# Optimization experiments

Measured on AMD Instinct MI355X. Metric: run time of the kernel, lower is better.

The kernel has to match this reference:

```python
import math
import jax, jax.numpy as jnp
import numpy as np

INPUT_DIM = 1024


def setup_inputs() -> dict:
    key = jax.random.key(0)
    k1, k2, k3 = jax.random.split(key, 3)
    x = jax.random.normal(k1, (16, INPUT_DIM, 64, 64), dtype=jnp.float32)
    # Conv2d(input_dim, 1, kernel_size=1): weight [1, C, 1, 1] -> store as [C], bias [1]
    fan_in = INPUT_DIM
    bound = 1.0 / math.sqrt(fan_in)
    key_w = jax.random.uniform(k2, (INPUT_DIM,), minval=-bound, maxval=bound, dtype=jnp.float32)
    key_b = jax.random.uniform(k3, (1,), minval=-bound, maxval=bound, dtype=jnp.float32)
    return {"x": x, "key_w": key_w, "key_b": key_b}


def reference(x, key_w, key_b):
    B, C, H, W = x.shape
    scale = 1.0 / math.sqrt(C)
    # 1x1 conv C->1 == channel contraction; logits over spatial positions
    logits = (jnp.einsum('bchw,c->bhw', x, key_w) + key_b[0]) * scale  # [B,H,W]
    attn = jax.nn.softmax(logits.reshape(B, H * W).astype(jnp.float32), axis=-1)  # [B,HW]
    rs_x = x.reshape(B, C, H * W)
    focus = jnp.einsum('bcs,bs->bc', rs_x, attn)  # weighted channel sum
    return focus.reshape(B, C, 1, 1)
```

## Files before the change

### kernel.cpp

```cpp
#include <hip/hip_runtime.h>
#include <math.h>

#define BB 16
#define CC 1024
#define SS 4096
#define SCH 16
#define KBLK (SS / SCH)

__device__ __forceinline__ float4 shfl_down_f4(float4 v, int d) {
    v.x = __shfl_down(v.x, d);
    v.y = __shfl_down(v.y, d);
    v.z = __shfl_down(v.z, d);
    v.w = __shfl_down(v.w, d);
    return v;
}
__device__ __forceinline__ void add4(float4& a, const float4 b) {
    a.x += b.x; a.y += b.y; a.z += b.z; a.w += b.w;
}

__global__ __launch_bounds__(512, 2) void k_fused(
    const float* __restrict__ x, const float* __restrict__ w,
    const float* __restrict__ bias,
    float* __restrict__ Nk, float* __restrict__ sk)
{
    __shared__ float4 wred[32];

    const int kblk = blockIdx.x;
    const int b    = blockIdx.y;
    const int t    = threadIdx.x;
    const int wave = t >> 6;
    const int lane = t & 63;
    const int q    = t >> 2;
    const int m    = t & 3;

    const float* xb = x + (size_t)b * CC * SS + (size_t)q * SS
                        + kblk * SCH + m * 4;

    float4 xv[8];
#pragma unroll
    for (int i = 0; i < 8; ++i)
        xv[i] = *(const float4*)(xb + (size_t)i * 128 * SS);

    float wreg[8];
#pragma unroll
    for (int i = 0; i < 8; ++i) wreg[i] = w[q + 128 * i];
    const float bv = bias[0];

    float4 lacc = make_float4(0.f, 0.f, 0.f, 0.f);
#pragma unroll
    for (int i = 0; i < 8; ++i) {
        lacc.x += xv[i].x * wreg[i];
        lacc.y += xv[i].y * wreg[i];
        lacc.z += xv[i].z * wreg[i];
        lacc.w += xv[i].w * wreg[i];
    }

    add4(lacc, shfl_down_f4(lacc, 4));
    add4(lacc, shfl_down_f4(lacc, 8));
    add4(lacc, shfl_down_f4(lacc, 16));
    add4(lacc, shfl_down_f4(lacc, 32));
    if (lane < 4) wred[wave * 4 + lane] = lacc;
    __syncthreads();

    float4 r0 = wred[ 0 + m];
    float4 r1 = wred[ 4 + m];
    add4(r0, wred[ 8 + m]);
    add4(r1, wred[12 + m]);
    add4(r0, wred[16 + m]);
    add4(r1, wred[20 + m]);
    add4(r0, wred[24 + m]);
    add4(r1, wred[28 + m]);
    add4(r0, r1);

    float4 e;
    e.x = __expf((r0.x + bv) * 0.03125f);
    e.y = __expf((r0.y + bv) * 0.03125f);
    e.z = __expf((r0.z + bv) * 0.03125f);
    e.w = __expf((r0.w + bv) * 0.03125f);

#pragma unroll
    for (int i = 0; i < 8; ++i) {
        float v = xv[i].x * e.x + xv[i].y * e.y
                + xv[i].z * e.z + xv[i].w * e.w;
        v += __shfl_down(v, 1);
        v += __shfl_down(v, 2);
        if (m == 0)
            Nk[((size_t)(b * KBLK + kblk)) * CC + q + 128 * i] = v;
    }

    if (t < 4) {
        float sv = (e.x + e.y) + (e.z + e.w);
        sv += __shfl_down(sv, 1);
        sv += __shfl_down(sv, 2);
        if (t == 0) sk[b * KBLK + kblk] = sv;
    }
}

__global__ __launch_bounds__(256) void k_combine(
    const float* __restrict__ Nk, const float* __restrict__ sk,
    float* __restrict__ out)
{
    __shared__ float part[4][64];

    const int b  = blockIdx.y;
    const int c0 = blockIdx.x * 64;
    const int t  = threadIdx.x;
    const int c  = t & 63;
    const int kg = t >> 6;

    float sv = 0.f;
#pragma unroll
    for (int j = 0; j < 4; ++j) sv += sk[b * KBLK + (t & 63) + 64 * j];
    for (int d = 32; d; d >>= 1) sv += __shfl_xor(sv, d);
    const float D = sv;

    float acc = 0.f;
    const float* Nb = Nk + (size_t)b * KBLK * CC + (size_t)(kg * 64) * CC + c0 + c;
#pragma unroll 8
    for (int j = 0; j < 64; ++j)
        acc += Nb[(size_t)j * CC];
    part[kg][c] = acc;
    __syncthreads();

    if (t < 64)
        out[b * CC + c0 + t] =
            (part[0][t] + part[1][t] + part[2][t] + part[3][t]) / D;
}

extern "C" void kernel_launch(void* const* d_in, const int* in_sizes, int n_in,
                              void* d_out, int out_size, void* d_ws, size_t ws_size,
                              hipStream_t stream) {
    const float* x    = (const float*)d_in[0];
    const float* w    = (const float*)d_in[1];
    const float* bias = (const float*)d_in[2];
    float* out = (float*)d_out;

    float* Nk = (float*)d_ws;
    float* sk = Nk + (size_t)BB * KBLK * CC;

    k_fused<<<dim3(KBLK, BB), 512, 0, stream>>>(x, w, bias, Nk, sk);
    k_combine<<<dim3(CC / 64, BB), 256, 0, stream>>>(Nk, sk, out);
}
```

Before: 382.8 us.

## Restructure fused kernel to per-wave channel ownership with chunked spatial loop

Each wave now owns all 1024 channels (16 per lane) and iterates over four spatial chunks, reducing logits with a full-wave xor shuffle instead of a shared-memory cross-wave reduction. Partial weighted sums accumulate in registers across chunks and are written once per wave, with a barrier per chunk to keep waves in lockstep on adjacent addresses. This removes LDS traffic and a syncthreads but lowers grid parallelism, raises register pressure, and makes each lane read a separate row.

```diff
diff --git a/kernel.cpp b/kernel.cpp
--- a/kernel.cpp
+++ b/kernel.cpp
@@ -4,96 +4,91 @@
 #define BB 16
 #define CC 1024
 #define SS 4096
-#define SCH 16
-#define KBLK (SS / SCH)
+#define WCH 4
+#define NCH 4
+#define WPB 4
+#define KBLK (SS / (WCH * NCH))
 
-__device__ __forceinline__ float4 shfl_down_f4(float4 v, int d) {
-    v.x = __shfl_down(v.x, d);
-    v.y = __shfl_down(v.y, d);
-    v.z = __shfl_down(v.z, d);
-    v.w = __shfl_down(v.w, d);
+__device__ __forceinline__ float4 shfl_xor_f4(float4 v, int d) {
+    v.x = __shfl_xor(v.x, d);
+    v.y = __shfl_xor(v.y, d);
+    v.z = __shfl_xor(v.z, d);
+    v.w = __shfl_xor(v.w, d);
     return v;
 }
 __device__ __forceinline__ void add4(float4& a, const float4 b) {
     a.x += b.x; a.y += b.y; a.z += b.z; a.w += b.w;
 }
 
-__global__ __launch_bounds__(512, 2) void k_fused(
+__global__ __launch_bounds__(256, 3) void k_fused(
     const float* __restrict__ x, const float* __restrict__ w,
     const float* __restrict__ bias,
     float* __restrict__ Nk, float* __restrict__ sk)
 {
-    __shared__ float4 wred[32];
-
-    const int kblk = blockIdx.x;
+    const int bx   = blockIdx.x;
     const int b    = blockIdx.y;
     const int t    = threadIdx.x;
-    const int wave = t >> 6;
+    const int wv   = t >> 6;
     const int lane = t & 63;
-    const int q    = t >> 2;
-    const int m    = t & 3;
+    const int wid  = bx * WPB + wv;
 
-    const float* xb = x + (size_t)b * CC * SS + (size_t)q * SS
-                        + kblk * SCH + m * 4;
+    const float* xr = x + (size_t)b * CC * SS + (size_t)lane * SS
+                        + bx * (WPB * NCH * WCH) + wv * WCH;
 
-    float4 xv[8];
+    float wreg[16];
 #pragma unroll
-    for (int i = 0; i < 8; ++i)
-        xv[i] = *(const float4*)(xb + (size_t)i * 128 * SS);
-
-    float wreg[8];
-#pragma unroll
-    for (int i = 0; i < 8; ++i) wreg[i] = w[q + 128 * i];
+    for (int i = 0; i < 16; ++i) wreg[i] = w[lane + 64 * i];
     const float bv = bias[0];
 
-    float4 lacc = make_float4(0.f, 0.f, 0.f, 0.f);
+    float np[16];
 #pragma unroll
-    for (int i = 0; i < 8; ++i) {
-        lacc.x += xv[i].x * wreg[i];
-        lacc.y += xv[i].y * wreg[i];
-        lacc.z += xv[i].z * wreg[i];
-        lacc.w += xv[i].w * wreg[i];
+    for (int i = 0; i < 16; ++i) np[i] = 0.f;
+    float s_part = 0.f;
+
+#pragma unroll
+    for (int ch = 0; ch < NCH; ++ch) {
+        float4 xv[16];
+#pragma unroll
+        for (int i = 0; i < 16; ++i)
+            xv[i] = *(const float4*)(xr + (size_t)i * 64 * SS
+                                        + ch * (WPB * WCH));
+
+        float4 lacc = make_float4(0.f, 0.f, 0.f, 0.f);
+#pragma unroll
+        for (int i = 0; i < 16; ++i) {
+            lacc.x += xv[i].x * wreg[i];
+            lacc.y += xv[i].y * wreg[i];
+            lacc.z += xv[i].z * wreg[i];
+            lacc.w += xv[i].w * wreg[i];
+        }
+
+        add4(lacc, shfl_xor_f4(lacc, 1));
+        add4(lacc, shfl_xor_f4(lacc, 2));
+        add4(lacc, shfl_xor_f4(lacc, 4));
+        add4(lacc, shfl_xor_f4(lacc, 8));
+        add4(lacc, shfl_xor_f4(lacc, 16));
+        add4(lacc, shfl_xor_f4(lacc, 32));
+
+        float4 e;
+        e.x = __expf((lacc.x + bv) * 0.03125f);
+        e.y = __expf((lacc.y + bv) * 0.03125f);
+        e.z = __expf((lacc.z + bv) * 0.03125f);
+        e.w = __expf((lacc.w + bv) * 0.03125f);
+        s_part += (e.x + e.y) + (e.z + e.w);
+
+#pragma unroll
+        for (int i = 0; i < 16; ++i)
+            np[i] += xv[i].x * e.x + xv[i].y * e.y
+                   + xv[i].z * e.z + xv[i].w * e.w;
+
+        __builtin_amdgcn_s_barrier();
     }
 
-    add4(lacc, shfl_down_f4(lacc, 4));
-    add4(lacc, shfl_down_f4(lacc, 8));
-    add4(lacc, shfl_down_f4(lacc, 16));
-    add4(lacc, shfl_down_f4(lacc, 32));
-    if (lane < 4) wred[wave * 4 + lane] = lacc;
-    __syncthreads();
-
-    float4 r0 = wred[ 0 + m];
-    float4 r1 = wred[ 4 + m];
-    add4(r0, wred[ 8 + m]);
-    add4(r1, wred[12 + m]);
-    add4(r0, wred[16 + m]);
-    add4(r1, wred[20 + m]);
-    add4(r0, wred[24 + m]);
-    add4(r1, wred[28 + m]);
-    add4(r0, r1);
-
-    float4 e;
-    e.x = __expf((r0.x + bv) * 0.03125f);
-    e.y = __expf((r0.y + bv) * 0.03125f);
-    e.z = __expf((r0.z + bv) * 0.03125f);
-    e.w = __expf((r0.w + bv) * 0.03125f);
-
+    float* NkRow = Nk + (size_t)(b * KBLK + wid) * CC;
 #pragma unroll
-    for (int i = 0; i < 8; ++i) {
-        float v = xv[i].x * e.x + xv[i].y * e.y
-                + xv[i].z * e.z + xv[i].w * e.w;
-        v += __shfl_down(v, 1);
-        v += __shfl_down(v, 2);
-        if (m == 0)
-            Nk[((size_t)(b * KBLK + kblk)) * CC + q + 128 * i] = v;
-    }
-
-    if (t < 4) {
-        float sv = (e.x + e.y) + (e.z + e.w);
-        sv += __shfl_down(sv, 1);
-        sv += __shfl_down(sv, 2);
-        if (t == 0) sk[b * KBLK + kblk] = sv;
-    }
+    for (int i = 0; i < 16; ++i)
+        NkRow[lane + 64 * i] = np[i];
+    if (lane == 0) sk[b * KBLK + wid] = s_part;
 }
 
 __global__ __launch_bounds__(256) void k_combine(
@@ -138,6 +133,7 @@
     float* Nk = (float*)d_ws;
     float* sk = Nk + (size_t)BB * KBLK * CC;
 
-    k_fused<<<dim3(KBLK, BB), 512, 0, stream>>>(x, w, bias, Nk, sk);
+    k_fused<<<dim3(SS / (WPB * NCH * WCH), BB), 256, 0, stream>>>(
+        x, w, bias, Nk, sk);
     k_combine<<<dim3(CC / 64, BB), 256, 0, stream>>>(Nk, sk, out);
 }
```

New measurement: 401.5 us. +4.9%, slower.
